# Kernel tuning notes

Hardware: AMD Instinct MI355X
Metric: run time of the kernel (lower is better)

## Reference

```python
import jax, jax.numpy as jnp
import numpy as np

B, H, W, C = 16, 56, 56, 256
NH, WS, SS = 8, 7, 3          # heads, window size, shift size
HD = C // NH                  # head dim = 32
MLPD = 4 * C                  # mlp hidden = 1024
WA = WS * WS                  # window area = 49
NW = (H // WS) * (W // WS)    # windows per image = 64
SCALE = HD ** -0.5


def _rel_pos_index():
    coords = np.stack(np.meshgrid(np.arange(WS), np.arange(WS), indexing='ij'))
    cf = coords.reshape(2, -1)
    rel = (cf[:, :, None] - cf[:, None, :]).transpose(1, 2, 0)
    rel[:, :, 0] += WS - 1
    rel[:, :, 1] += WS - 1
    rel[:, :, 0] *= 2 * WS - 1
    return rel.sum(-1)  # (WA, WA) int


def _shift_attn_mask():
    img = np.zeros((H, W))
    cnt = 0
    for hs in (slice(0, -WS), slice(-WS, -SS), slice(-SS, None)):
        for ws_ in (slice(0, -WS), slice(-WS, -SS), slice(-SS, None)):
            img[hs, ws_] = cnt
            cnt += 1
    mw = img.reshape(H // WS, WS, W // WS, WS).transpose(0, 2, 1, 3).reshape(-1, WA)
    am = mw[:, None, :] - mw[:, :, None]
    return np.where(am != 0, -100.0, 0.0).astype(np.float32)  # (NW, WA, WA)

REL_IDX = jnp.asarray(_rel_pos_index())
ATTN_MASK = jnp.asarray(_shift_attn_mask())


def setup_inputs() -> dict:
    key = jax.random.key(0)
    ks = jax.random.split(key, 8)
    s = 0.02
    return {
        'x':      jax.random.normal(ks[0], (B, H * W, C), jnp.float32),
        'g1':     jnp.ones((C,), jnp.float32),
        'be1':    jnp.zeros((C,), jnp.float32),
        'w_qkv':  jax.random.normal(ks[1], (C, 3 * C), jnp.float32) * s,
        'b_qkv':  jnp.zeros((3 * C,), jnp.float32),
        'rpt':    jax.random.normal(ks[2], ((2 * WS - 1) ** 2, NH), jnp.float32) * s,
        'w_proj': jax.random.normal(ks[3], (C, C), jnp.float32) * s,
        'b_proj': jnp.zeros((C,), jnp.float32),
        'g2':     jnp.ones((C,), jnp.float32),
        'be2':    jnp.zeros((C,), jnp.float32),
        'w_fc1':  jax.random.normal(ks[4], (C, MLPD), jnp.float32) * s,
        'b_fc1':  jnp.zeros((MLPD,), jnp.float32),
        'w_fc2':  jax.random.normal(ks[5], (MLPD, C), jnp.float32) * s,
        'b_fc2':  jnp.zeros((C,), jnp.float32),
    }


def _ln(x, g, b, eps=1e-5):
    m = x.mean(-1, keepdims=True)
    v = ((x - m) ** 2).mean(-1, keepdims=True)
    return (x - m) * jax.lax.rsqrt(v + eps) * g + b


def reference(x, g1, be1, w_qkv, b_qkv, rpt, w_proj, b_proj, g2, be2,
              w_fc1, b_fc1, w_fc2, b_fc2):
    shortcut = x
    h = _ln(x, g1, be1).reshape(B, H, W, C)
    # cyclic shift
    h = jnp.roll(h, (-SS, -SS), axis=(1, 2))
    # window partition -> (B*NW, WA, C)
    h = h.reshape(B, H // WS, WS, W // WS, WS, C).transpose(0, 1, 3, 2, 4, 5)
    h = h.reshape(B * NW, WA, C)
    # qkv
    qkv = h @ w_qkv + b_qkv                       # (B*NW, WA, 3C)
    qkv = qkv.reshape(B * NW, WA, 3, NH, HD).transpose(2, 0, 3, 1, 4)
    q, k, v = qkv[0], qkv[1], qkv[2]              # (B*NW, NH, WA, HD)
    attn = jnp.einsum('wnqd,wnkd->wnqk', q * SCALE, k)   # (B*NW, NH, WA, WA)
    # relative position bias
    bias = rpt[REL_IDX.reshape(-1)].reshape(WA, WA, NH).transpose(2, 0, 1)
    attn = attn + bias[None]
    # shifted-window mask, per window
    attn = attn.reshape(B, NW, NH, WA, WA) + ATTN_MASK[None, :, None]
    attn = jax.nn.softmax(attn.reshape(B * NW, NH, WA, WA), axis=-1)
    out = jnp.einsum('wnqk,wnkd->wnqd', attn, v)  # (B*NW, NH, WA, HD)
    out = out.transpose(0, 2, 1, 3).reshape(B * NW, WA, C)
    out = out @ w_proj + b_proj
    # window reverse + unshift
    out = out.reshape(B, H // WS, W // WS, WS, WS, C).transpose(0, 1, 3, 2, 4, 5)
    out = out.reshape(B, H, W, C)
    out = jnp.roll(out, (SS, SS), axis=(1, 2)).reshape(B, H * W, C)
    x = shortcut + out
    # MLP block
    h2 = _ln(x, g2, be2)
    h2 = jax.nn.gelu(h2 @ w_fc1 + b_fc1, approximate=False) @ w_fc2 + b_fc2
    return x + h2
```

## Files before the change

kernel.cpp:

```cpp
#include <hip/hip_runtime.h>
#include <hip/hip_bf16.h>
#include <cstdint>
#include <cstddef>
#include <type_traits>

typedef __attribute__((ext_vector_type(8))) short short8;
typedef __attribute__((ext_vector_type(4))) float f32x4;
typedef __attribute__((ext_vector_type(4))) unsigned short us4;

#define DEVINL __device__ __forceinline__

static constexpr int SS_ = 3;
static constexpr int HH = 56, WW = 56;
#define SCALE_Q 0.17677669529663689f

DEVINL unsigned short f2b(float f) {
    unsigned int u = __builtin_bit_cast(unsigned int, f);
    unsigned int r = (u + 0x7FFFu + ((u >> 16) & 1u)) >> 16;
    return (unsigned short)r;
}
DEVINL float b2f(unsigned short s) {
    return __builtin_bit_cast(float, ((unsigned int)s) << 16);
}

DEVINL float gelu(float v) {
    float ax = fabsf(v) * 0.70710678118654752f;
    float t = 1.0f / (1.0f + 0.47047f * ax);
    float poly = t * (0.3480242f + t * (-0.0958798f + t * 0.7478556f));
    float erfv = 1.0f - poly * __expf(-ax * ax);
    erfv = v >= 0.0f ? erfv : -erfv;
    return 0.5f * v * (1.0f + erfv);
}

DEVINL void gload_lds16(const unsigned short* g, unsigned short* l) {
    __builtin_amdgcn_global_load_lds(
        (const __attribute__((address_space(1))) unsigned int*)g,
        (__attribute__((address_space(3))) unsigned int*)l, 16, 0, 0);
}

__global__ void wconv_kernel(const float* __restrict__ in,
                             unsigned short* __restrict__ out, int K, int N) {
    int i = blockIdx.x * 256 + threadIdx.x;
    if (i >= K * N) return;
    int k = i / N, n = i - k * N;
    out[(size_t)n * K + k] = f2b(in[i]);
}

template <int MODE, typename TIN>
__global__ __launch_bounds__(256) void ln_kernel(
    const TIN* __restrict__ x, const float* __restrict__ g,
    const float* __restrict__ be, unsigned short* __restrict__ out) {
    const int wid = threadIdx.x >> 6, lane = threadIdx.x & 63;
    const int t = blockIdx.x * 4 + wid;
    int src;
    if constexpr (MODE == 1) {
        int w = t / 49, p = t - w * 49;
        int b = w >> 6, widx = w & 63;
        int wy = widx >> 3, wx = widx & 7;
        int py = p / 7, px = p - py * 7;
        int y = wy * 7 + py + SS_;  if (y >= HH) y -= HH;
        int xx = wx * 7 + px + SS_; if (xx >= WW) xx -= WW;
        src = b * (HH * WW) + y * WW + xx;
    } else {
        src = t;
    }
    float4 v;
    if constexpr (std::is_same_v<TIN, float>) {
        v = reinterpret_cast<const float4*>(x + (size_t)src * 256)[lane];
    } else {
        us4 u = reinterpret_cast<const us4*>(x + (size_t)src * 256)[lane];
        v.x = b2f(u.x); v.y = b2f(u.y); v.z = b2f(u.z); v.w = b2f(u.w);
    }
    float s = v.x + v.y + v.z + v.w;
    float q = v.x * v.x + v.y * v.y + v.z * v.z + v.w * v.w;
#pragma unroll
    for (int m = 1; m < 64; m <<= 1) {
        s += __shfl_xor(s, m);
        q += __shfl_xor(q, m);
    }
    float mean = s * (1.0f / 256.0f);
    float var = q * (1.0f / 256.0f) - mean * mean;
    float rs = rsqrtf(var + 1e-5f);
    int c = lane * 4;
    us4 o;
    o.x = f2b((v.x - mean) * rs * g[c + 0] + be[c + 0]);
    o.y = f2b((v.y - mean) * rs * g[c + 1] + be[c + 1]);
    o.z = f2b((v.z - mean) * rs * g[c + 2] + be[c + 2]);
    o.w = f2b((v.w - mean) * rs * g[c + 3] + be[c + 3]);
    *reinterpret_cast<us4*>(out + (size_t)t * 256 + c) = o;
}

template <int KDIM, int EPI>
__global__ __launch_bounds__(256, 4) void gemm_kernel(
    const unsigned short* __restrict__ A, const unsigned short* __restrict__ Bt,
    const float* __restrict__ bias, void* __restrict__ out0,
    const void* __restrict__ res, unsigned short* __restrict__ o_q,
    unsigned short* __restrict__ o_k, unsigned short* __restrict__ o_v) {
    constexpr int BM = 128, BN = 128, BK = 64;
    __shared__ __align__(16) unsigned short As[BM * BK];
    __shared__ __align__(16) unsigned short Bs[BN * BK];
    const int tid = threadIdx.x;
    const int wid = tid >> 6, lane = tid & 63;

    const int nwg = gridDim.x * gridDim.y;
    const int bid = blockIdx.x + gridDim.x * blockIdx.y;
    const int nb = (bid & 7) * (nwg >> 3) + (bid >> 3);
    const int n0 = (nb % gridDim.x) * BN;
    const int m0 = (nb / gridDim.x) * BM;

    const int wm = wid >> 1, wn = wid & 1;
    const int lr = lane & 15, kg = lane >> 4;
    f32x4 acc[4][4] = {};

    const int srow = tid >> 3;
    const int spos = tid & 7;

    for (int kt = 0; kt < KDIM; kt += BK) {
#pragma unroll
        for (int i = 0; i < 4; i++) {
            int row = i * 32 + srow;
            gload_lds16(A + (size_t)(m0 + row) * KDIM + kt + ((spos ^ (row & 7)) << 3),
                        As + i * 2048 + tid * 8);
        }
#pragma unroll
        for (int i = 0; i < 4; i++) {
            int row = i * 32 + srow;
            gload_lds16(Bt + (size_t)(n0 + row) * KDIM + kt + ((spos ^ (row & 7)) << 3),
                        Bs + i * 2048 + tid * 8);
        }
        __syncthreads();
#pragma unroll
        for (int ks = 0; ks < 2; ks++) {
            short8 a[4], b[4];
#pragma unroll
            for (int mf = 0; mf < 4; mf++) {
                int r = wm * 64 + mf * 16 + lr;
                a[mf] = *reinterpret_cast<const short8*>(
                    As + r * 64 + (((ks * 4 + kg) ^ (r & 7)) << 3));
            }
#pragma unroll
            for (int nf = 0; nf < 4; nf++) {
                int r = wn * 64 + nf * 16 + lr;
                b[nf] = *reinterpret_cast<const short8*>(
                    Bs + r * 64 + (((ks * 4 + kg) ^ (r & 7)) << 3));
            }
#pragma unroll
            for (int mf = 0; mf < 4; mf++)
#pragma unroll
                for (int nf = 0; nf < 4; nf++)
                    acc[mf][nf] = __builtin_amdgcn_mfma_f32_16x16x32_bf16(
                        a[mf], b[nf], acc[mf][nf], 0, 0, 0);
        }
        __syncthreads();
    }

    if constexpr (EPI == 2) {
        __shared__ unsigned short eps_s[128 * 136];
#pragma unroll
        for (int mf = 0; mf < 4; mf++) {
#pragma unroll
            for (int nf = 0; nf < 4; nf++) {
                int col_l = wn * 64 + nf * 16 + lr;
                float bq = bias[n0 + col_l];
#pragma unroll
                for (int j = 0; j < 4; j++) {
                    int row_l = wm * 64 + mf * 16 + kg * 4 + j;
                    eps_s[row_l * 136 + col_l] = f2b(gelu(acc[mf][nf][j] + bq));
                }
            }
        }
        __syncthreads();
        unsigned short* outp = (unsigned short*)out0;
        const int r_l = tid >> 4, c_l = (tid & 15) * 8;
#pragma unroll
        for (int i = 0; i < 8; i++) {
            int r = i * 16 + r_l;
            short8 v = *reinterpret_cast<const short8*>(eps_s + r * 136 + c_l);
            *reinterpret_cast<short8*>(outp + (size_t)(m0 + r) * 1024 + n0 + c_l) = v;
        }
        return;
    }

#pragma unroll
    for (int mf = 0; mf < 4; mf++) {
#pragma unroll
        for (int nf = 0; nf < 4; nf++) {
#pragma unroll
            for (int j = 0; j < 4; j++) {
                int row = m0 + wm * 64 + mf * 16 + kg * 4 + j;
                int col = n0 + wn * 64 + nf * 16 + lr;
                float v = acc[mf][nf][j] + bias[col];
                if constexpr (EPI == 0) {
                    int w = row / 49, p = row - w * 49;
                    int which = col >> 8, h = (col >> 5) & 7, d = col & 31;
                    size_t th = (size_t)(w * 8 + h);
                    if (which == 0)
                        o_q[th * 1568 + p * 32 + d] = f2b(v * SCALE_Q);
                    else if (which == 1)
                        o_k[th * 1568 + p * 32 + d] = f2b(v);
                    else
                        o_v[th * 2048 + d * 64 + p] = f2b(v);
                } else if constexpr (EPI == 1) {
                    int w = row / 49, p = row - w * 49;
                    int b2 = w >> 6, widx = w & 63;
                    int wy = widx >> 3, wx = widx & 7;
                    int py = p / 7, px = p - py * 7;
                    int y = wy * 7 + py + SS_;  if (y >= HH) y -= HH;
                    int xx = wx * 7 + px + SS_; if (xx >= WW) xx -= WW;
                    size_t oi = ((size_t)(b2 * 3136 + y * 56 + xx)) * 256 + col;
                    reinterpret_cast<unsigned short*>(out0)[oi] =
                        f2b(v + reinterpret_cast<const float*>(res)[oi]);
                } else {
                    size_t oi = (size_t)row * 256 + col;
                    reinterpret_cast<float*>(out0)[oi] =
                        v + b2f(reinterpret_cast<const unsigned short*>(res)[oi]);
                }
            }
        }
    }
}

__global__ __launch_bounds__(256) void attn_kernel(
    const unsigned short* __restrict__ qg, const unsigned short* __restrict__ kgl,
    const unsigned short* __restrict__ vg, const float* __restrict__ rpt,
    unsigned short* __restrict__ out) {
    __shared__ __align__(16) unsigned short sm[4][6144];
    __shared__ unsigned short rpts[169 * 8];
    const int tid = threadIdx.x, wid = tid >> 6, lane = tid & 63;
    for (int i = tid; i < 169 * 8; i += 256) rpts[i] = f2b(rpt[i]);
    const int task = blockIdx.x * 4 + wid;
    const int w = task >> 3, h = task & 7;
    const int widx = w & 63, wy = widx >> 3, wx = widx & 7;
    unsigned short* q_s = sm[wid];
    unsigned short* k_s = sm[wid] + 2048;
    unsigned short* v_s = sm[wid] + 4096;
    unsigned short* p_s = sm[wid];
    const unsigned short* qsrc = qg + (size_t)task * 1568;
    const unsigned short* ksrc = kgl + (size_t)task * 1568;
    const unsigned short* vsrc = vg + (size_t)task * 2048;
    for (int c = lane; c < 196; c += 64) {
        int row = c >> 2, kc = c & 3;
        int off = (row * 32 + kc * 8) ^ ((row & 7) << 3);
        *reinterpret_cast<short8*>(q_s + off) =
            *reinterpret_cast<const short8*>(qsrc + c * 8);
        *reinterpret_cast<short8*>(k_s + off) =
            *reinterpret_cast<const short8*>(ksrc + c * 8);
    }
#pragma unroll
    for (int i = 0; i < 4; i++) {
        int c = i * 64 + lane;
        int row = c >> 3, kc = c & 7;
        int off = (row * 64 + kc * 8) ^ ((row & 7) << 3);
        *reinterpret_cast<short8*>(v_s + off) =
            *reinterpret_cast<const short8*>(vsrc + c * 8);
    }
    __syncthreads();

    const int lr = lane & 15, kg = lane >> 4;
    short8 af[4], bf[4];
#pragma unroll
    for (int mf = 0; mf < 4; mf++) {
        int r = mf * 16 + lr;
        af[mf] = *reinterpret_cast<const short8*>(
            q_s + ((r * 32 + kg * 8) ^ ((r & 7) << 3)));
    }
#pragma unroll
    for (int nf = 0; nf < 4; nf++) {
        int r = nf * 16 + lr;
        bf[nf] = *reinterpret_cast<const short8*>(
            k_s + ((r * 32 + kg * 8) ^ ((r & 7) << 3)));
    }
    f32x4 s[4][4] = {};
#pragma unroll
    for (int mf = 0; mf < 4; mf++)
#pragma unroll
        for (int nf = 0; nf < 4; nf++)
            s[mf][nf] = __builtin_amdgcn_mfma_f32_16x16x32_bf16(af[mf], bf[nf],
                                                                s[mf][nf], 0, 0, 0);
#pragma unroll
    for (int mf = 0; mf < 4; mf++) {
#pragma unroll
        for (int j = 0; j < 4; j++) {
            int row = mf * 16 + kg * 4 + j;
            bool rvalid = row < 49;
            int qy = 0, qx = 0, gq = 0;
            if (rvalid) {
                qy = row / 7; qx = row - qy * 7;
                int yi = wy * 7 + qy, xi = wx * 7 + qx;
                gq = ((yi < 49) ? 0 : ((yi < 53) ? 1 : 2)) * 3 +
                     ((xi < 49) ? 0 : ((xi < 53) ? 1 : 2));
            }
            float L[4];
#pragma unroll
            for (int nf = 0; nf < 4; nf++) {
                int col = nf * 16 + lr;
                float val = s[mf][nf][j];
                if (rvalid && col < 49) {
                    int ky = col / 7, kx = col - ky * 7;
                    int yi = wy * 7 + ky, xi = wx * 7 + kx;
                    int gk = ((yi < 49) ? 0 : ((yi < 53) ? 1 : 2)) * 3 +
                             ((xi < 49) ? 0 : ((xi < 53) ? 1 : 2));
                    val += b2f(rpts[((qy - ky + 6) * 13 + (qx - kx + 6)) * 8 + h]);
                    if (gq != gk) val -= 100.0f;
                } else {
                    val = -1e30f;
                }
                L[nf] = val;
            }
            float m = fmaxf(fmaxf(L[0], L[1]), fmaxf(L[2], L[3]));
#pragma unroll
            for (int t2 = 1; t2 < 16; t2 <<= 1) m = fmaxf(m, __shfl_xor(m, t2));
            float P[4], psum = 0.f;
#pragma unroll
            for (int nf = 0; nf < 4; nf++) {
                P[nf] = __expf(L[nf] - m);
                psum += P[nf];
            }
#pragma unroll
            for (int t2 = 1; t2 < 16; t2 <<= 1) psum += __shfl_xor(psum, t2);
            float inv = 1.0f / psum;
#pragma unroll
            for (int nf = 0; nf < 4; nf++) {
                int col = nf * 16 + lr;
                p_s[(row * 64 + col) ^ ((row & 7) << 3)] = f2b(P[nf] * inv);
            }
        }
    }
    f32x4 o[4][2] = {};
#pragma unroll
    for (int ks = 0; ks < 2; ks++) {
        short8 pa[4], vb[2];
#pragma unroll
        for (int mf = 0; mf < 4; mf++) {
            int r = mf * 16 + lr;
            pa[mf] = *reinterpret_cast<const short8*>(
                p_s + ((r * 64 + ks * 32 + kg * 8) ^ ((r & 7) << 3)));
        }
#pragma unroll
        for (int nf = 0; nf < 2; nf++) {
            int d = nf * 16 + lr;
            vb[nf] = *reinterpret_cast<const short8*>(
                v_s + ((d * 64 + ks * 32 + kg * 8) ^ ((d & 7) << 3)));
        }
#pragma unroll
        for (int mf = 0; mf < 4; mf++)
#pragma unroll
            for (int nf = 0; nf < 2; nf++)
                o[mf][nf] = __builtin_amdgcn_mfma_f32_16x16x32_bf16(
                    pa[mf], vb[nf], o[mf][nf], 0, 0, 0);
    }
#pragma unroll
    for (int mf = 0; mf < 4; mf++) {
#pragma unroll
        for (int j = 0; j < 4; j++) {
            int row = mf * 16 + kg * 4 + j;
            if (row < 49) {
#pragma unroll
                for (int nf = 0; nf < 2; nf++) {
                    int d = nf * 16 + lr;
                    out[((size_t)w * 49 + row) * 256 + h * 32 + d] =
                        f2b(o[mf][nf][j]);
                }
            }
        }
    }
}

extern "C" void kernel_launch(void* const* d_in, const int* in_sizes, int n_in,
                              void* d_out, int out_size, void* d_ws,
                              size_t ws_size, hipStream_t stream) {
    const float* x     = (const float*)d_in[0];
    const float* g1    = (const float*)d_in[1];
    const float* be1   = (const float*)d_in[2];
    const float* wqkv  = (const float*)d_in[3];
    const float* bqkv  = (const float*)d_in[4];
    const float* rpt   = (const float*)d_in[5];
    const float* wproj = (const float*)d_in[6];
    const float* bproj = (const float*)d_in[7];
    const float* g2    = (const float*)d_in[8];
    const float* be2   = (const float*)d_in[9];
    const float* wfc1  = (const float*)d_in[10];
    const float* bfc1  = (const float*)d_in[11];
    const float* wfc2  = (const float*)d_in[12];
    const float* bfc2  = (const float*)d_in[13];
    float* out = (float*)d_out;
    char* ws = (char*)d_ws;

    unsigned short* hb  = (unsigned short*)(ws);
    unsigned short* qg  = (unsigned short*)(ws + 25690112);
    unsigned short* kgl = (unsigned short*)(ws + 51380224);
    unsigned short* vg  = (unsigned short*)(ws + 77070336);
    unsigned short* x2b = (unsigned short*)(ws + 110624768);
    unsigned short* h2  = (unsigned short*)(ws + 162004992);
    unsigned short* wT  = (unsigned short*)(ws + 187695104);
    unsigned short* wqkvT = wT;
    unsigned short* wprojT = wT + 196608;
    unsigned short* wfc1T  = wT + 262144;
    unsigned short* wfc2T  = wT + 524288;
    unsigned short* a1 = (unsigned short*)ws;

    wconv_kernel<<<(256 * 768 + 255) / 256, 256, 0, stream>>>(wqkv, wqkvT, 256, 768);
    wconv_kernel<<<(256 * 256 + 255) / 256, 256, 0, stream>>>(wproj, wprojT, 256, 256);
    wconv_kernel<<<(256 * 1024 + 255) / 256, 256, 0, stream>>>(wfc1, wfc1T, 256, 1024);
    wconv_kernel<<<(1024 * 256 + 255) / 256, 256, 0, stream>>>(wfc2, wfc2T, 1024, 256);

    ln_kernel<1, float><<<12544, 256, 0, stream>>>(x, g1, be1, hb);
    gemm_kernel<256, 0><<<dim3(6, 392), 256, 0, stream>>>(
        hb, wqkvT, bqkv, nullptr, nullptr, qg, kgl, vg);
    attn_kernel<<<2048, 256, 0, stream>>>(qg, kgl, vg, rpt, hb);
    gemm_kernel<256, 1><<<dim3(2, 392), 256, 0, stream>>>(
        hb, wprojT, bproj, x2b, x, nullptr, nullptr, nullptr);
    ln_kernel<0, unsigned short><<<12544, 256, 0, stream>>>(x2b, g2, be2, h2);
    gemm_kernel<256, 2><<<dim3(8, 392), 256, 0, stream>>>(
        h2, wfc1T, bfc1, a1, nullptr, nullptr, nullptr, nullptr);
    gemm_kernel<1024, 3><<<dim3(2, 392), 256, 0, stream>>>(
        a1, wfc2T, bfc2, out, x2b, nullptr, nullptr, nullptr);
}
```

Before: 295.8 us.

## Fuse MLP fc1+GELU and fc2 into one kernel keeping hidden activations in LDS

Replaces the two MLP GEMM launches with one fused kernel. Each 512-thread block computes a 64-row tile of fc1+GELU into a 128KB shared-memory buffer with XOR swizzling, then runs fc2 from that buffer and adds the bias and residual. This removes the global-memory round trip of the 1024-wide hidden activation and one launch. In exchange the fused kernel reads its operands straight from global memory with no LDS staging or double buffering, and the large LDS footprint limits it to about one block per CU, so latency hiding may suffer.

```diff
diff --git a/kernel.cpp b/kernel.cpp
--- a/kernel.cpp
+++ b/kernel.cpp
@@ -154,33 +154,6 @@
         __syncthreads();
     }
 
-    if constexpr (EPI == 2) {
-        __shared__ unsigned short eps_s[128 * 136];
-#pragma unroll
-        for (int mf = 0; mf < 4; mf++) {
-#pragma unroll
-            for (int nf = 0; nf < 4; nf++) {
-                int col_l = wn * 64 + nf * 16 + lr;
-                float bq = bias[n0 + col_l];
-#pragma unroll
-                for (int j = 0; j < 4; j++) {
-                    int row_l = wm * 64 + mf * 16 + kg * 4 + j;
-                    eps_s[row_l * 136 + col_l] = f2b(gelu(acc[mf][nf][j] + bq));
-                }
-            }
-        }
-        __syncthreads();
-        unsigned short* outp = (unsigned short*)out0;
-        const int r_l = tid >> 4, c_l = (tid & 15) * 8;
-#pragma unroll
-        for (int i = 0; i < 8; i++) {
-            int r = i * 16 + r_l;
-            short8 v = *reinterpret_cast<const short8*>(eps_s + r * 136 + c_l);
-            *reinterpret_cast<short8*>(outp + (size_t)(m0 + r) * 1024 + n0 + c_l) = v;
-        }
-        return;
-    }
-
 #pragma unroll
     for (int mf = 0; mf < 4; mf++) {
 #pragma unroll
@@ -200,7 +173,7 @@
                         o_k[th * 1568 + p * 32 + d] = f2b(v);
                     else
                         o_v[th * 2048 + d * 64 + p] = f2b(v);
-                } else if constexpr (EPI == 1) {
+                } else {
                     int w = row / 49, p = row - w * 49;
                     int b2 = w >> 6, widx = w & 63;
                     int wy = widx >> 3, wx = widx & 7;
@@ -210,11 +183,101 @@
                     size_t oi = ((size_t)(b2 * 3136 + y * 56 + xx)) * 256 + col;
                     reinterpret_cast<unsigned short*>(out0)[oi] =
                         f2b(v + reinterpret_cast<const float*>(res)[oi]);
-                } else {
-                    size_t oi = (size_t)row * 256 + col;
-                    reinterpret_cast<float*>(out0)[oi] =
-                        v + b2f(reinterpret_cast<const unsigned short*>(res)[oi]);
                 }
+            }
+        }
+    }
+}
+
+__global__ __launch_bounds__(512) void fc_fused_kernel(
+    const unsigned short* __restrict__ h2,
+    const unsigned short* __restrict__ w1t,
+    const float* __restrict__ b1,
+    const unsigned short* __restrict__ w2t,
+    const float* __restrict__ b2,
+    const unsigned short* __restrict__ res,
+    float* __restrict__ out) {
+    __shared__ __align__(16) unsigned short a1s[64 * 1024];
+    const int tid = threadIdx.x;
+    const int wid = tid >> 6, lane = tid & 63;
+    const int lr = lane & 15, kg = lane >> 4;
+    const int m0 = blockIdx.x * 64;
+
+#pragma unroll 1
+    for (int p = 0; p < 2; p++) {
+        const int nbase = wid * 128 + p * 64;
+        f32x4 acc[4][4] = {};
+#pragma unroll
+        for (int ks = 0; ks < 8; ks++) {
+            short8 hf[4], wf[4];
+#pragma unroll
+            for (int mf = 0; mf < 4; mf++)
+                hf[mf] = *reinterpret_cast<const short8*>(
+                    h2 + (size_t)(m0 + mf * 16 + lr) * 256 + ks * 32 + kg * 8);
+#pragma unroll
+            for (int nf = 0; nf < 4; nf++)
+                wf[nf] = *reinterpret_cast<const short8*>(
+                    w1t + (size_t)(nbase + nf * 16 + lr) * 256 + ks * 32 + kg * 8);
+#pragma unroll
+            for (int mf = 0; mf < 4; mf++)
+#pragma unroll
+                for (int nf = 0; nf < 4; nf++)
+                    acc[mf][nf] = __builtin_amdgcn_mfma_f32_16x16x32_bf16(
+                        wf[nf], hf[mf], acc[mf][nf], 0, 0, 0);
+        }
+#pragma unroll
+        for (int nf = 0; nf < 4; nf++) {
+            const int ncol = nbase + nf * 16 + kg * 4;
+            const float4 bq = *reinterpret_cast<const float4*>(b1 + ncol);
+            const int c8 = ncol >> 3, woff = ncol & 7;
+#pragma unroll
+            for (int mf = 0; mf < 4; mf++) {
+                const int row = mf * 16 + lr;
+                us4 o;
+                o.x = f2b(gelu(acc[mf][nf][0] + bq.x));
+                o.y = f2b(gelu(acc[mf][nf][1] + bq.y));
+                o.z = f2b(gelu(acc[mf][nf][2] + bq.z));
+                o.w = f2b(gelu(acc[mf][nf][3] + bq.w));
+                *reinterpret_cast<us4*>(
+                    a1s + row * 1024 + ((c8 ^ (row & 7)) << 3) + woff) = o;
+            }
+        }
+    }
+    __syncthreads();
+
+    const int wm2 = wid >> 2, wn2 = wid & 3;
+    f32x4 acc2[2][4] = {};
+#pragma unroll 4
+    for (int kt = 0; kt < 32; kt++) {
+        short8 af[2], bf[4];
+#pragma unroll
+        for (int mf = 0; mf < 2; mf++) {
+            const int m = wm2 * 32 + mf * 16 + lr;
+            af[mf] = *reinterpret_cast<const short8*>(
+                a1s + m * 1024 + (((kt * 4 + kg) ^ (m & 7)) << 3));
+        }
+#pragma unroll
+        for (int nf = 0; nf < 4; nf++)
+            bf[nf] = *reinterpret_cast<const short8*>(
+                w2t + (size_t)(wn2 * 64 + nf * 16 + lr) * 1024 + kt * 32 + kg * 8);
+#pragma unroll
+        for (int mf = 0; mf < 2; mf++)
+#pragma unroll
+            for (int nf = 0; nf < 4; nf++)
+                acc2[mf][nf] = __builtin_amdgcn_mfma_f32_16x16x32_bf16(
+                    af[mf], bf[nf], acc2[mf][nf], 0, 0, 0);
+    }
+#pragma unroll
+    for (int nf = 0; nf < 4; nf++) {
+        const int col = wn2 * 64 + nf * 16 + lr;
+        const float bb = b2[col];
+#pragma unroll
+        for (int mf = 0; mf < 2; mf++) {
+#pragma unroll
+            for (int j = 0; j < 4; j++) {
+                const int row = m0 + wm2 * 32 + mf * 16 + kg * 4 + j;
+                const size_t oi = (size_t)row * 256 + col;
+                out[oi] = acc2[mf][nf][j] + bb + b2f(res[oi]);
             }
         }
     }
@@ -397,7 +460,6 @@
     unsigned short* wprojT = wT + 196608;
     unsigned short* wfc1T  = wT + 262144;
     unsigned short* wfc2T  = wT + 524288;
-    unsigned short* a1 = (unsigned short*)ws;
 
     wconv_kernel<<<(256 * 768 + 255) / 256, 256, 0, stream>>>(wqkv, wqkvT, 256, 768);
     wconv_kernel<<<(256 * 256 + 255) / 256, 256, 0, stream>>>(wproj, wprojT, 256, 256);
@@ -411,8 +473,6 @@
     gemm_kernel<256, 1><<<dim3(2, 392), 256, 0, stream>>>(
         hb, wprojT, bproj, x2b, x, nullptr, nullptr, nullptr);
     ln_kernel<0, unsigned short><<<12544, 256, 0, stream>>>(x2b, g2, be2, h2);
-    gemm_kernel<256, 2><<<dim3(8, 392), 256, 0, stream>>>(
-        h2, wfc1T, bfc1, a1, nullptr, nullptr, nullptr, nullptr);
-    gemm_kernel<1024, 3><<<dim3(2, 392), 256, 0, stream>>>(
-        a1, wfc2T, bfc2, out, x2b, nullptr, nullptr, nullptr);
-}
+    fc_fused_kernel<<<784, 512, 0, stream>>>(
+        h2, wfc1T, bfc1, wfc2T, bfc2, x2b, out);
+}
```

Result: slower. 436.5 us (+47.6%).

## Add K=256 GEMM kernel keeping B tile resident across four M tiles

Applied to the files above, without the earlier changes.

Adds a specialized GEMM for K=256 that loads the whole 128x256 weight tile into LDS once and loops over four consecutive 128-row M tiles, staging A per K-slice and overlapping the next tile's first A load with the epilogue. The grid shrinks by 4x in M, and the XCD remap now handles non-multiple-of-8 counts. The goal is to cut repeated weight loads and launch/prologue cost for the QKV, proj and FC1 GEMMs. In exchange it uses more LDS (occupancy 2), has fewer workgroups, and drops the LDS-staged coalesced store for the GELU epilogue in favor of direct scattered stores.

```diff
diff --git a/kernel.cpp b/kernel.cpp
--- a/kernel.cpp
+++ b/kernel.cpp
@@ -90,6 +90,131 @@
     *reinterpret_cast<us4*>(out + (size_t)t * 256 + c) = o;
 }
 
+template <int EPI>
+__global__ __launch_bounds__(256, 2) void gemm_k256_kernel(
+    const unsigned short* __restrict__ A, const unsigned short* __restrict__ Bt,
+    const float* __restrict__ bias, void* __restrict__ out0,
+    const void* __restrict__ res, unsigned short* __restrict__ o_q,
+    unsigned short* __restrict__ o_k, unsigned short* __restrict__ o_v) {
+    __shared__ __align__(16) unsigned short Bs[4][8192];
+    __shared__ __align__(16) unsigned short As[8192];
+    const int tid = threadIdx.x;
+    const int wid = tid >> 6, lane = tid & 63;
+
+    const int nwg = gridDim.x * gridDim.y;
+    const int orig = blockIdx.x + gridDim.x * blockIdx.y;
+    const int q8 = nwg >> 3, r8 = nwg & 7;
+    const int xcd = orig & 7, idx = orig >> 3;
+    const int nb = (xcd < r8 ? xcd * (q8 + 1) : r8 * (q8 + 1) + (xcd - r8) * q8) + idx;
+    const int n0 = (nb % gridDim.x) * 128;
+    const int mg = nb / gridDim.x;
+
+    const int wm = wid >> 1, wn = wid & 1;
+    const int lr = lane & 15, kg = lane >> 4;
+    const int srow = tid >> 3, spos = tid & 7;
+
+    auto stageA = [&](int m0, int kt) {
+#pragma unroll
+        for (int i = 0; i < 4; i++) {
+            int row = i * 32 + srow;
+            gload_lds16(A + (size_t)(m0 + row) * 256 + kt * 64 +
+                            ((spos ^ (row & 7)) << 3),
+                        As + i * 2048 + tid * 8);
+        }
+    };
+
+#pragma unroll
+    for (int kt = 0; kt < 4; kt++)
+#pragma unroll
+        for (int i = 0; i < 4; i++) {
+            int row = i * 32 + srow;
+            gload_lds16(Bt + (size_t)(n0 + row) * 256 + kt * 64 +
+                            ((spos ^ (row & 7)) << 3),
+                        Bs[kt] + i * 2048 + tid * 8);
+        }
+    stageA(mg * 512, 0);
+    __syncthreads();
+
+#pragma unroll 1
+    for (int g = 0; g < 4; g++) {
+        const int m0 = mg * 512 + g * 128;
+        f32x4 acc[4][4] = {};
+
+        auto epilogue = [&]() {
+#pragma unroll
+            for (int mf = 0; mf < 4; mf++) {
+#pragma unroll
+                for (int nf = 0; nf < 4; nf++) {
+#pragma unroll
+                    for (int j = 0; j < 4; j++) {
+                        int row = m0 + wm * 64 + mf * 16 + kg * 4 + j;
+                        int col = n0 + wn * 64 + nf * 16 + lr;
+                        float v = acc[mf][nf][j] + bias[col];
+                        if constexpr (EPI == 0) {
+                            int w = row / 49, p = row - w * 49;
+                            int which = col >> 8, h = (col >> 5) & 7, d = col & 31;
+                            size_t th = (size_t)(w * 8 + h);
+                            if (which == 0)
+                                o_q[th * 1568 + p * 32 + d] = f2b(v * SCALE_Q);
+                            else if (which == 1)
+                                o_k[th * 1568 + p * 32 + d] = f2b(v);
+                            else
+                                o_v[th * 2048 + d * 64 + p] = f2b(v);
+                        } else if constexpr (EPI == 1) {
+                            int w = row / 49, p = row - w * 49;
+                            int b2 = w >> 6, widx = w & 63;
+                            int wy = widx >> 3, wx = widx & 7;
+                            int py = p / 7, px = p - py * 7;
+                            int y = wy * 7 + py + SS_;  if (y >= HH) y -= HH;
+                            int xx = wx * 7 + px + SS_; if (xx >= WW) xx -= WW;
+                            size_t oi = ((size_t)(b2 * 3136 + y * 56 + xx)) * 256 + col;
+                            reinterpret_cast<unsigned short*>(out0)[oi] =
+                                f2b(v + reinterpret_cast<const float*>(res)[oi]);
+                        } else {
+                            reinterpret_cast<unsigned short*>(out0)
+                                [(size_t)row * 1024 + col] = f2b(gelu(v));
+                        }
+                    }
+                }
+            }
+        };
+
+#pragma unroll
+        for (int kt = 0; kt < 4; kt++) {
+#pragma unroll
+            for (int ks = 0; ks < 2; ks++) {
+                short8 a[4], b[4];
+#pragma unroll
+                for (int mf = 0; mf < 4; mf++) {
+                    int r = wm * 64 + mf * 16 + lr;
+                    a[mf] = *reinterpret_cast<const short8*>(
+                        As + r * 64 + (((ks * 4 + kg) ^ (r & 7)) << 3));
+                }
+#pragma unroll
+                for (int nf = 0; nf < 4; nf++) {
+                    int r = wn * 64 + nf * 16 + lr;
+                    b[nf] = *reinterpret_cast<const short8*>(
+                        Bs[kt] + r * 64 + (((ks * 4 + kg) ^ (r & 7)) << 3));
+                }
+#pragma unroll
+                for (int mf = 0; mf < 4; mf++)
+#pragma unroll
+                    for (int nf = 0; nf < 4; nf++)
+                        acc[mf][nf] = __builtin_amdgcn_mfma_f32_16x16x32_bf16(
+                            a[mf], b[nf], acc[mf][nf], 0, 0, 0);
+            }
+            __syncthreads();
+            if (kt < 3) {
+                stageA(m0, kt + 1);
+            } else {
+                if (g < 3) stageA(m0 + 128, 0);
+                epilogue();
+            }
+            __syncthreads();
+        }
+    }
+}
+
 template <int KDIM, int EPI>
 __global__ __launch_bounds__(256, 4) void gemm_kernel(
     const unsigned short* __restrict__ A, const unsigned short* __restrict__ Bt,
@@ -154,33 +279,6 @@
         __syncthreads();
     }
 
-    if constexpr (EPI == 2) {
-        __shared__ unsigned short eps_s[128 * 136];
-#pragma unroll
-        for (int mf = 0; mf < 4; mf++) {
-#pragma unroll
-            for (int nf = 0; nf < 4; nf++) {
-                int col_l = wn * 64 + nf * 16 + lr;
-                float bq = bias[n0 + col_l];
-#pragma unroll
-                for (int j = 0; j < 4; j++) {
-                    int row_l = wm * 64 + mf * 16 + kg * 4 + j;
-                    eps_s[row_l * 136 + col_l] = f2b(gelu(acc[mf][nf][j] + bq));
-                }
-            }
-        }
-        __syncthreads();
-        unsigned short* outp = (unsigned short*)out0;
-        const int r_l = tid >> 4, c_l = (tid & 15) * 8;
-#pragma unroll
-        for (int i = 0; i < 8; i++) {
-            int r = i * 16 + r_l;
-            short8 v = *reinterpret_cast<const short8*>(eps_s + r * 136 + c_l);
-            *reinterpret_cast<short8*>(outp + (size_t)(m0 + r) * 1024 + n0 + c_l) = v;
-        }
-        return;
-    }
-
 #pragma unroll
     for (int mf = 0; mf < 4; mf++) {
 #pragma unroll
@@ -190,31 +288,9 @@
                 int row = m0 + wm * 64 + mf * 16 + kg * 4 + j;
                 int col = n0 + wn * 64 + nf * 16 + lr;
                 float v = acc[mf][nf][j] + bias[col];
-                if constexpr (EPI == 0) {
-                    int w = row / 49, p = row - w * 49;
-                    int which = col >> 8, h = (col >> 5) & 7, d = col & 31;
-                    size_t th = (size_t)(w * 8 + h);
-                    if (which == 0)
-                        o_q[th * 1568 + p * 32 + d] = f2b(v * SCALE_Q);
-                    else if (which == 1)
-                        o_k[th * 1568 + p * 32 + d] = f2b(v);
-                    else
-                        o_v[th * 2048 + d * 64 + p] = f2b(v);
-                } else if constexpr (EPI == 1) {
-                    int w = row / 49, p = row - w * 49;
-                    int b2 = w >> 6, widx = w & 63;
-                    int wy = widx >> 3, wx = widx & 7;
-                    int py = p / 7, px = p - py * 7;
-                    int y = wy * 7 + py + SS_;  if (y >= HH) y -= HH;
-                    int xx = wx * 7 + px + SS_; if (xx >= WW) xx -= WW;
-                    size_t oi = ((size_t)(b2 * 3136 + y * 56 + xx)) * 256 + col;
-                    reinterpret_cast<unsigned short*>(out0)[oi] =
-                        f2b(v + reinterpret_cast<const float*>(res)[oi]);
-                } else {
-                    size_t oi = (size_t)row * 256 + col;
-                    reinterpret_cast<float*>(out0)[oi] =
-                        v + b2f(reinterpret_cast<const unsigned short*>(res)[oi]);
-                }
+                size_t oi = (size_t)row * 256 + col;
+                reinterpret_cast<float*>(out0)[oi] =
+                    v + b2f(reinterpret_cast<const unsigned short*>(res)[oi]);
             }
         }
     }
@@ -405,13 +481,13 @@
     wconv_kernel<<<(1024 * 256 + 255) / 256, 256, 0, stream>>>(wfc2, wfc2T, 1024, 256);
 
     ln_kernel<1, float><<<12544, 256, 0, stream>>>(x, g1, be1, hb);
-    gemm_kernel<256, 0><<<dim3(6, 392), 256, 0, stream>>>(
+    gemm_k256_kernel<0><<<dim3(6, 98), 256, 0, stream>>>(
         hb, wqkvT, bqkv, nullptr, nullptr, qg, kgl, vg);
     attn_kernel<<<2048, 256, 0, stream>>>(qg, kgl, vg, rpt, hb);
-    gemm_kernel<256, 1><<<dim3(2, 392), 256, 0, stream>>>(
+    gemm_k256_kernel<1><<<dim3(2, 98), 256, 0, stream>>>(
         hb, wprojT, bproj, x2b, x, nullptr, nullptr, nullptr);
     ln_kernel<0, unsigned short><<<12544, 256, 0, stream>>>(x2b, g2, be2, h2);
-    gemm_kernel<256, 2><<<dim3(8, 392), 256, 0, stream>>>(
+    gemm_k256_kernel<2><<<dim3(8, 98), 256, 0, stream>>>(
         h2, wfc1T, bfc1, a1, nullptr, nullptr, nullptr, nullptr);
     gemm_kernel<1024, 3><<<dim3(2, 392), 256, 0, stream>>>(
         a1, wfc2T, bfc2, out, x2b, nullptr, nullptr, nullptr);
```

Result: slower. 322.2 us (+8.9%).
